# Performance work log

Measured on AMD Instinct MI355X. Metric: run time of the kernel, lower is better.

Reference implementation:

```python
import jax, jax.numpy as jnp
import numpy as np

B, S, D, H, F = 2, 2048, 1024, 16, 64  # batch, seq, d_model, heads, head_dim


def setup_inputs() -> dict:
    key = jax.random.key(0)
    ks = jax.random.split(key, 7)
    return {
        "q": jax.random.normal(ks[0], (B, S, D), dtype=jnp.float32),
        "k": jax.random.normal(ks[1], (B, S, D), dtype=jnp.float32),
        "v": jax.random.normal(ks[2], (B, S, D), dtype=jnp.float32),
        "Wq": jax.random.normal(ks[3], (H, D, F), dtype=jnp.float32) * 0.02,
        "Wk": jax.random.normal(ks[4], (H, D, F), dtype=jnp.float32) * 0.02,
        "Wv": jax.random.normal(ks[5], (H, D, F), dtype=jnp.float32) * 0.02,
        "Wo": jax.random.normal(ks[6], (H * F, D), dtype=jnp.float32) * 0.02,
    }


def reference(q, k, v, Wq, Wk, Wv, Wo):
    head_dim = Wq.shape[-1]
    queries = jnp.einsum('bqo,hof->bhqf', q, Wq)
    keys = jnp.einsum('bko,hof->bhkf', k, Wk)
    values = jnp.einsum('bvo,hof->bhvf', v, Wv)
    # K.batch_dot(queries, keys, axes=[3,3]) -> [b,h,q,k]
    scores = jnp.einsum('bhqf,bhkf->bhqk', queries, keys) / jnp.sqrt(
        jnp.asarray(head_dim, dtype=queries.dtype))
    attn = jax.nn.softmax(scores, axis=-1)
    # Faithful to K.batch_dot(attn, values, axes=[2,2]):
    # contracts the QUERY axis of attn with the seq axis of values -> A^T V
    out4 = jnp.einsum('bhqk,bhqf->bhkf', attn, values)  # [b,h,s,f]
    b = out4.shape[0]
    # Faithful raw reshape [b,h,s,f] -> [b,s,h*f] (no transpose, as in original)
    out = out4.reshape(b, out4.shape[2], -1)
    return out @ Wo  # [b,s,d_model]
```

## Files before the change

### kernel.cpp

```cpp
#include <hip/hip_runtime.h>
#include <stdint.h>

#define Bc 2
#define Sc 2048
#define Dc 1024
#define Hc 16
#define Fc 64
constexpr int BHSF = Bc * Hc * Sc * Fc;

typedef __attribute__((ext_vector_type(8))) short bf16x8;
typedef __attribute__((ext_vector_type(4))) short bf16x4;
typedef __attribute__((ext_vector_type(4))) float f32x4;

#define MFMA16(a, b, c) __builtin_amdgcn_mfma_f32_16x16x32_bf16(a, b, c, 0, 0, 0)
#define EXP2(x) __builtin_amdgcn_exp2f(x)
#define SCALE2 0.18033688f

__device__ inline short f2bf(float x) {
    uint32_t u = __builtin_bit_cast(uint32_t, x);
    u = (u + 0x7fffu + ((u >> 16) & 1u)) >> 16;
    return (short)u;
}

__global__ __launch_bounds__(256) void xcvt_kernel(
    const float* __restrict__ a, const float* __restrict__ b,
    const float* __restrict__ c, short* __restrict__ out)
{
    const float* src = (blockIdx.y == 0) ? a : (blockIdx.y == 1) ? b : c;
    const size_t base = (size_t)blockIdx.x * 4096 + threadIdx.x * 16;
    const float* s = src + base;
    short* d = out + (size_t)blockIdx.y * 4096 * 1024 + base;
    f32x4 v0 = ((const f32x4*)s)[0], v1 = ((const f32x4*)s)[1];
    f32x4 v2 = ((const f32x4*)s)[2], v3 = ((const f32x4*)s)[3];
    bf16x8 p0, p1;
    #pragma unroll
    for (int i = 0; i < 4; ++i) {
        p0[i] = f2bf(v0[i]); p0[4 + i] = f2bf(v1[i]);
        p1[i] = f2bf(v2[i]); p1[4 + i] = f2bf(v3[i]);
    }
    *(bf16x8*)d       = p0;
    *(bf16x8*)(d + 8) = p1;
}

__global__ __launch_bounds__(256) void tcvt3_kernel(
    const float* __restrict__ Wq, const float* __restrict__ Wk,
    const float* __restrict__ Wv,
    short* __restrict__ WqT, short* __restrict__ WkT, short* __restrict__ WvT)
{
    __shared__ short td[64 * 72];
    const int t = threadIdx.x;
    const int sr = t >> 2, sc = (t & 3) * 16;
    const int sel = blockIdx.z >> 4, h = blockIdx.z & 15;
    const int m0 = blockIdx.x * 64;
    const float* in = ((sel == 0) ? Wq : (sel == 1) ? Wk : Wv) + (size_t)h * Dc * Fc;
    short* out = ((sel == 0) ? WqT : (sel == 1) ? WkT : WvT) + (size_t)h * Fc * Dc;

    const float* src = in + (size_t)(m0 + sr) * Fc + sc;
    #pragma unroll
    for (int i = 0; i < 16; i += 4) {
        f32x4 a = *(const f32x4*)(src + i);
        td[sr * 72 + sc + i + 0] = f2bf(a[0]);
        td[sr * 72 + sc + i + 1] = f2bf(a[1]);
        td[sr * 72 + sc + i + 2] = f2bf(a[2]);
        td[sr * 72 + sc + i + 3] = f2bf(a[3]);
    }
    __syncthreads();
    alignas(16) short vals[16];
    #pragma unroll
    for (int i = 0; i < 16; ++i) vals[i] = td[(sc + i) * 72 + sr];
    short* dst = out + (size_t)sr * Dc + m0 + sc;
    *(bf16x8*)dst       = *(const bf16x8*)&vals[0];
    *(bf16x8*)(dst + 8) = *(const bf16x8*)&vals[8];
}

__global__ __launch_bounds__(256) void tcvt_kernel(
    const float* __restrict__ in, short* __restrict__ out, int M, int N)
{
    __shared__ short td[64 * 72];
    const int t = threadIdx.x;
    const int sr = t >> 2, sc = (t & 3) * 16;
    const int m0 = blockIdx.x * 64, n0 = blockIdx.y * 64;

    const float* src = in + (size_t)(m0 + sr) * N + n0 + sc;
    #pragma unroll
    for (int i = 0; i < 16; i += 4) {
        f32x4 a = *(const f32x4*)(src + i);
        td[sr * 72 + sc + i + 0] = f2bf(a[0]);
        td[sr * 72 + sc + i + 1] = f2bf(a[1]);
        td[sr * 72 + sc + i + 2] = f2bf(a[2]);
        td[sr * 72 + sc + i + 3] = f2bf(a[3]);
    }
    __syncthreads();
    alignas(16) short vals[16];
    #pragma unroll
    for (int i = 0; i < 16; ++i) vals[i] = td[(sc + i) * 72 + sr];
    short* dst = out + (size_t)(n0 + sr) * M + m0 + sc;
    *(bf16x8*)dst       = *(const bf16x8*)&vals[0];
    *(bf16x8*)(dst + 8) = *(const bf16x8*)&vals[8];
}

__global__ __launch_bounds__(256) void proj_kernel(
    const short* __restrict__ Xb,
    const short* __restrict__ WqT, const short* __restrict__ WkT,
    const short* __restrict__ WvT,
    short* __restrict__ Qo, short* __restrict__ Ko, short* __restrict__ VtO)
{
    const int z = blockIdx.z, h = blockIdx.x, mt = blockIdx.y;
    const short* X  = Xb + (size_t)z * 4096 * Dc;
    const short* Wt = ((z == 0) ? WqT : (z == 1) ? WkT : WvT) + (size_t)h * Fc * Dc;
    const int m0 = mt * 128;

    __shared__ short xsA[128 * 72], xsB[128 * 72];
    __shared__ short wsA[64 * 72],  wsB[64 * 72];

    const int t = threadIdx.x, lane = t & 63, w = t >> 6;
    const int l15 = lane & 15, g = lane >> 4;
    const int xr = t >> 1, xc = (t & 1) * 32;
    const int wr = t >> 2, wc = (t & 3) * 16;

    bf16x8 xg[4], wg[2];
    auto gload = [&](int d0) {
        const short* s = &X[(size_t)(m0 + xr) * Dc + d0 + xc];
        #pragma unroll
        for (int j = 0; j < 4; ++j) xg[j] = *(const bf16x8*)(s + 8 * j);
        const short* ww = &Wt[(size_t)wr * Dc + d0 + wc];
        wg[0] = *(const bf16x8*)ww;
        wg[1] = *(const bf16x8*)(ww + 8);
    };
    auto swrite = [&](short* xsD, short* wsD) {
        #pragma unroll
        for (int j = 0; j < 4; ++j) *(bf16x8*)&xsD[xr * 72 + xc + 8 * j] = xg[j];
        *(bf16x8*)&wsD[wr * 72 + wc]     = wg[0];
        *(bf16x8*)&wsD[wr * 72 + wc + 8] = wg[1];
    };

    f32x4 acc[2][4];
    #pragma unroll
    for (int i = 0; i < 2; ++i)
        #pragma unroll
        for (int j = 0; j < 4; ++j) acc[i][j] = (f32x4){0.f, 0.f, 0.f, 0.f};

    gload(0); swrite(xsA, wsA); gload(64);

    auto half = [&](int d0, const short* xsC, const short* wsC,
                    short* xsN, short* wsN) {
        __syncthreads();
        if (d0 + 64 < Dc) swrite(xsN, wsN);
        if (d0 + 128 < Dc) gload(d0 + 128);
        #pragma unroll
        for (int kc = 0; kc < 64; kc += 32) {
            bf16x8 afr[2], bfr[4];
            #pragma unroll
            for (int ms = 0; ms < 2; ++ms)
                afr[ms] = *(const bf16x8*)&xsC[(w * 32 + ms * 16 + l15) * 72 + kc + g * 8];
            #pragma unroll
            for (int fb = 0; fb < 4; ++fb)
                bfr[fb] = *(const bf16x8*)&wsC[(fb * 16 + l15) * 72 + kc + g * 8];
            #pragma unroll
            for (int ms = 0; ms < 2; ++ms)
                #pragma unroll
                for (int fb = 0; fb < 4; ++fb)
                    acc[ms][fb] = MFMA16(afr[ms], bfr[fb], acc[ms][fb]);
        }
    };

    for (int d0 = 0; d0 < Dc; d0 += 128) {
        half(d0,      xsA, wsA, xsB, wsB);
        half(d0 + 64, xsB, wsB, xsA, wsA);
    }

    __syncthreads();
    #pragma unroll
    for (int ms = 0; ms < 2; ++ms)
        #pragma unroll
        for (int fb = 0; fb < 4; ++fb)
            #pragma unroll
            for (int r = 0; r < 4; ++r)
                xsA[(w * 32 + ms * 16 + g * 4 + r) * 72 + fb * 16 + l15] =
                    f2bf(acc[ms][fb][r]);
    __syncthreads();

    const int b = m0 >> 11, s0 = m0 & 2047;
    if (z < 2) {
        short* outp = ((z == 0) ? Qo : Ko) + ((size_t)(b * Hc + h) * Sc + s0) * Fc;
        #pragma unroll
        for (int j = 0; j < 4; ++j)
            *(bf16x8*)&outp[(size_t)xr * Fc + xc + 8 * j] =
                *(const bf16x8*)&xsA[xr * 72 + xc + 8 * j];
    } else {
        const int fr = t >> 2, sc0 = (t & 3) * 32;
        short* o = VtO + ((size_t)(b * Hc + h) * Fc + fr) * Sc + s0 + sc0;
        alignas(16) short vals[32];
        #pragma unroll
        for (int j = 0; j < 32; ++j) vals[j] = xsA[(sc0 + j) * 72 + fr];
        #pragma unroll
        for (int j = 0; j < 4; ++j)
            *(bf16x8*)(o + 8 * j) = *(const bf16x8*)&vals[8 * j];
    }
}

__global__ __launch_bounds__(256) void stats_kernel(
    const short* __restrict__ Qg, const short* __restrict__ Kg,
    float* __restrict__ mrow)
{
    const int q0 = blockIdx.x * 128;
    const int bh = blockIdx.y;
    const short* Qb = Qg + (size_t)bh * Sc * Fc;
    const short* Kb = Kg + (size_t)bh * Sc * Fc;

    __shared__ short ksA[64 * 72], ksB[64 * 72];

    const int t = threadIdx.x, lane = t & 63, w = t >> 6;
    const int l15 = lane & 15, g = lane >> 4;
    const int sr4 = t >> 2, sc4 = (t & 3) * 16;

    bf16x8 qf[2][2];
    #pragma unroll
    for (int qs2 = 0; qs2 < 2; ++qs2)
        #pragma unroll
        for (int kc2 = 0; kc2 < 2; ++kc2)
            qf[qs2][kc2] = *(const bf16x8*)
                &Qb[(size_t)(q0 + w * 32 + qs2 * 16 + l15) * Fc + kc2 * 32 + g * 8];

    bf16x8 kr0, kr1;
    auto gload = [&](int kt) {
        const short* s = &Kb[(size_t)(kt + sr4) * Fc + sc4];
        kr0 = *(const bf16x8*)s;
        kr1 = *(const bf16x8*)(s + 8);
    };
    auto swrite = [&](short* d) {
        *(bf16x8*)&d[sr4 * 72 + sc4]     = kr0;
        *(bf16x8*)&d[sr4 * 72 + sc4 + 8] = kr1;
    };

    float m[2] = {-1e30f, -1e30f}, l[2] = {0.f, 0.f};

    gload(0); swrite(ksA); gload(64);

    auto half = [&](int kt, const short* cur, short* nxt) {
        __syncthreads();
        if (kt + 64 < Sc) swrite(nxt);
        if (kt + 128 < Sc) gload(kt + 128);
        #pragma unroll
        for (int kf = 0; kf < 4; ++kf) {
            bf16x8 a0 = *(const bf16x8*)&cur[(kf * 16 + l15) * 72 + 0  + g * 8];
            bf16x8 a1 = *(const bf16x8*)&cur[(kf * 16 + l15) * 72 + 32 + g * 8];
            #pragma unroll
            for (int qs2 = 0; qs2 < 2; ++qs2) {
                f32x4 acc = (f32x4){0.f, 0.f, 0.f, 0.f};
                acc = MFMA16(a0, qf[qs2][0], acc);
                acc = MFMA16(a1, qf[qs2][1], acc);
                float s0 = acc[0] * SCALE2, s1 = acc[1] * SCALE2;
                float s2 = acc[2] * SCALE2, s3 = acc[3] * SCALE2;
                float tm = fmaxf(fmaxf(s0, s1), fmaxf(s2, s3));
                float mn = fmaxf(m[qs2], tm);
                l[qs2] = l[qs2] * EXP2(m[qs2] - mn) + EXP2(s0 - mn) + EXP2(s1 - mn)
                                                    + EXP2(s2 - mn) + EXP2(s3 - mn);
                m[qs2] = mn;
            }
        }
    };

    for (int kt = 0; kt < Sc; kt += 128) {
        half(kt,      ksA, ksB);
        half(kt + 64, ksB, ksA);
    }

    #pragma unroll
    for (int qs2 = 0; qs2 < 2; ++qs2) {
        #pragma unroll
        for (int off = 16; off < 64; off <<= 1) {
            float om = __shfl_xor(m[qs2], off, 64);
            float ol = __shfl_xor(l[qs2], off, 64);
            float mn = fmaxf(m[qs2], om);
            l[qs2] = l[qs2] * EXP2(m[qs2] - mn) + ol * EXP2(om - mn);
            m[qs2] = mn;
        }
        if (lane < 16)
            mrow[bh * Sc + q0 + w * 32 + qs2 * 16 + l15] = m[qs2] + __log2f(l[qs2]);
    }
}

__global__ __launch_bounds__(256) void attn_kernel(
    const short* __restrict__ Qg, const short* __restrict__ Kg,
    const short* __restrict__ VtG, const float* __restrict__ mrow,
    short* __restrict__ O4)
{
    const int k0 = blockIdx.x * 128;
    const int bh = blockIdx.y;
    const short* Qb = Qg  + (size_t)bh * Sc * Fc;
    const short* Kb = Kg  + (size_t)bh * Sc * Fc;
    const short* Vb = VtG + (size_t)bh * Fc * Sc;
    const float* mb = mrow + (size_t)bh * Sc;

    __shared__ short qsA[64 * 72], qsB[64 * 72];
    __shared__ short vtA[64 * 72], vtB[64 * 72];
    __shared__ short pl[128 * 72];

    const int t = threadIdx.x, lane = t & 63, w = t >> 6;
    const int l15 = lane & 15, g = lane >> 4;
    const int sr4 = t >> 2, sc4 = (t & 3) * 16;

    bf16x8 kf[2][2];
    #pragma unroll
    for (int ks2 = 0; ks2 < 2; ++ks2)
        #pragma unroll
        for (int kc2 = 0; kc2 < 2; ++kc2)
            kf[ks2][kc2] = *(const bf16x8*)
                &Kb[(size_t)(k0 + w * 32 + ks2 * 16 + l15) * Fc + kc2 * 32 + g * 8];

    f32x4 oacc[2][4];
    #pragma unroll
    for (int i = 0; i < 2; ++i)
        #pragma unroll
        for (int j = 0; j < 4; ++j) oacc[i][j] = (f32x4){0.f, 0.f, 0.f, 0.f};

    bf16x8 qr0, qr1, vr0, vr1;
    auto gload = [&](int qn) {
        const short* s = &Qb[(size_t)(qn + sr4) * Fc + sc4];
        qr0 = *(const bf16x8*)s;
        qr1 = *(const bf16x8*)(s + 8);
        const short* v = &Vb[(size_t)sr4 * Sc + qn + sc4];
        vr0 = *(const bf16x8*)v;
        vr1 = *(const bf16x8*)(v + 8);
    };
    auto swrite = [&](short* qsD, short* vtD) {
        *(bf16x8*)&qsD[sr4 * 72 + sc4]     = qr0;
        *(bf16x8*)&qsD[sr4 * 72 + sc4 + 8] = qr1;
        *(bf16x8*)&vtD[sr4 * 72 + sc4]     = vr0;
        *(bf16x8*)&vtD[sr4 * 72 + sc4 + 8] = vr1;
    };

    gload(0); swrite(qsA, vtA); gload(64);

    auto chunk = [&](int q0, const short* qsC, const short* vtC,
                     short* qsN, short* vtN) {
        __syncthreads();
        if (q0 + 64 < Sc) swrite(qsN, vtN);
        if (q0 + 128 < Sc) gload(q0 + 128);

        f32x4 mq[4];
        #pragma unroll
        for (int qf = 0; qf < 4; ++qf)
            mq[qf] = *(const f32x4*)&mb[q0 + qf * 16 + g * 4];
        #pragma unroll
        for (int qf = 0; qf < 4; ++qf) {
            bf16x8 qa0 = *(const bf16x8*)&qsC[(qf * 16 + l15) * 72 + 0  + g * 8];
            bf16x8 qa1 = *(const bf16x8*)&qsC[(qf * 16 + l15) * 72 + 32 + g * 8];
            #pragma unroll
            for (int ks2 = 0; ks2 < 2; ++ks2) {
                f32x4 acc = (f32x4){0.f, 0.f, 0.f, 0.f};
                acc = MFMA16(qa0, kf[ks2][0], acc);
                acc = MFMA16(qa1, kf[ks2][1], acc);
                bf16x4 pv;
                #pragma unroll
                for (int r = 0; r < 4; ++r)
                    pv[r] = f2bf(EXP2(acc[r] * SCALE2 - mq[qf][r]));
                *(bf16x4*)&pl[(w * 32 + ks2 * 16 + l15) * 72 + qf * 16 + g * 4] = pv;
            }
        }
        __syncthreads();

        #pragma unroll
        for (int qc = 0; qc < 64; qc += 32) {
            bf16x8 pa[2], vbf[4];
            #pragma unroll
            for (int ks2 = 0; ks2 < 2; ++ks2)
                pa[ks2] = *(const bf16x8*)&pl[(w * 32 + ks2 * 16 + l15) * 72 + qc + g * 8];
            #pragma unroll
            for (int fb = 0; fb < 4; ++fb)
                vbf[fb] = *(const bf16x8*)&vtC[(fb * 16 + l15) * 72 + qc + g * 8];
            #pragma unroll
            for (int ks2 = 0; ks2 < 2; ++ks2)
                #pragma unroll
                for (int fb = 0; fb < 4; ++fb)
                    oacc[ks2][fb] = MFMA16(pa[ks2], vbf[fb], oacc[ks2][fb]);
        }
    };

    for (int q0 = 0; q0 < Sc; q0 += 128) {
        chunk(q0,      qsA, vtA, qsB, vtB);
        chunk(q0 + 64, qsB, vtB, qsA, vtA);
    }

    __syncthreads();
    #pragma unroll
    for (int ks2 = 0; ks2 < 2; ++ks2)
        #pragma unroll
        for (int fb = 0; fb < 4; ++fb)
            #pragma unroll
            for (int r = 0; r < 4; ++r)
                pl[(w * 32 + ks2 * 16 + g * 4 + r) * 72 + fb * 16 + l15] =
                    f2bf(oacc[ks2][fb][r]);
    __syncthreads();
    {
        const int sr2 = t >> 1, sc2 = (t & 1) * 32;
        short* o = O4 + ((size_t)bh * Sc + k0 + sr2) * Fc + sc2;
        #pragma unroll
        for (int i = 0; i < 32; i += 8)
            *(bf16x8*)&o[i] = *(const bf16x8*)&pl[sr2 * 72 + sc2 + i];
    }
}

__global__ __launch_bounds__(256) void outgemm_kernel(
    const short* __restrict__ A, const short* __restrict__ WoT,
    float* __restrict__ out)
{
    const int m0 = blockIdx.x * 128, n0 = blockIdx.y * 64;

    __shared__ short asA[128 * 72], asB[128 * 72];
    __shared__ short wsA[64 * 72],  wsB[64 * 72];

    const int t = threadIdx.x, lane = t & 63, w = t >> 6;
    const int l15 = lane & 15, g = lane >> 4;
    const int ar = t >> 1, ac = (t & 1) * 32;
    const int wr = t >> 2, wc = (t & 3) * 16;

    bf16x8 ag[4], wg[2];
    auto gload = [&](int d0) {
        const short* s = &A[(size_t)(m0 + ar) * Dc + d0 + ac];
        #pragma unroll
        for (int j = 0; j < 4; ++j) ag[j] = *(const bf16x8*)(s + 8 * j);
        const short* ww = &WoT[(size_t)(n0 + wr) * Dc + d0 + wc];
        wg[0] = *(const bf16x8*)ww;
        wg[1] = *(const bf16x8*)(ww + 8);
    };
    auto swrite = [&](short* asD, short* wsD) {
        #pragma unroll
        for (int j = 0; j < 4; ++j) *(bf16x8*)&asD[ar * 72 + ac + 8 * j] = ag[j];
        *(bf16x8*)&wsD[wr * 72 + wc]     = wg[0];
        *(bf16x8*)&wsD[wr * 72 + wc + 8] = wg[1];
    };

    f32x4 acc[2][4];
    #pragma unroll
    for (int i = 0; i < 2; ++i)
        #pragma unroll
        for (int j = 0; j < 4; ++j) acc[i][j] = (f32x4){0.f, 0.f, 0.f, 0.f};

    gload(0); swrite(asA, wsA); gload(64);

    auto half = [&](int d0, const short* asC, const short* wsC,
                    short* asN, short* wsN) {
        __syncthreads();
        if (d0 + 64 < Dc) swrite(asN, wsN);
        if (d0 + 128 < Dc) gload(d0 + 128);
        #pragma unroll
        for (int kc = 0; kc < 64; kc += 32) {
            bf16x8 afr[2], bfr[4];
            #pragma unroll
            for (int ms = 0; ms < 2; ++ms)
                afr[ms] = *(const bf16x8*)&asC[(w * 32 + ms * 16 + l15) * 72 + kc + g * 8];
            #pragma unroll
            for (int nb = 0; nb < 4; ++nb)
                bfr[nb] = *(const bf16x8*)&wsC[(nb * 16 + l15) * 72 + kc + g * 8];
            #pragma unroll
            for (int ms = 0; ms < 2; ++ms)
                #pragma unroll
                for (int nb = 0; nb < 4; ++nb)
                    acc[ms][nb] = MFMA16(afr[ms], bfr[nb], acc[ms][nb]);
        }
    };

    for (int d0 = 0; d0 < Dc; d0 += 128) {
        half(d0,      asA, wsA, asB, wsB);
        half(d0 + 64, asB, wsB, asA, wsA);
    }

    #pragma unroll
    for (int ms = 0; ms < 2; ++ms)
        #pragma unroll
        for (int nb = 0; nb < 4; ++nb)
            #pragma unroll
            for (int r = 0; r < 4; ++r)
                out[(size_t)(m0 + w * 32 + ms * 16 + g * 4 + r) * 1024
                    + n0 + nb * 16 + l15] = acc[ms][nb][r];
}

extern "C" void kernel_launch(void* const* d_in, const int* in_sizes, int n_in,
                              void* d_out, int out_size, void* d_ws, size_t ws_size,
                              hipStream_t stream) {
    (void)in_sizes; (void)n_in; (void)out_size; (void)ws_size;
    const float* q  = (const float*)d_in[0];
    const float* k  = (const float*)d_in[1];
    const float* v  = (const float*)d_in[2];
    const float* Wq = (const float*)d_in[3];
    const float* Wk = (const float*)d_in[4];
    const float* Wv = (const float*)d_in[5];
    const float* Wo = (const float*)d_in[6];
    float* out = (float*)d_out;

    short* Xb  = (short*)d_ws;
    short* Qw  = Xb  + (size_t)3 * 4096 * Dc;
    short* Kw  = Qw  + BHSF;
    short* Vt  = Kw  + BHSF;
    short* O4  = Vt  + BHSF;
    short* WqT = O4  + BHSF;
    short* WkT = WqT + Hc * Dc * Fc;
    short* WvT = WkT + Hc * Dc * Fc;
    short* WoT = WvT + Hc * Dc * Fc;
    float* mw  = (float*)(WoT + Dc * Dc);

    xcvt_kernel<<<dim3(1024, 3), 256, 0, stream>>>(q, k, v, Xb);
    tcvt3_kernel<<<dim3(16, 1, 48), 256, 0, stream>>>(Wq, Wk, Wv, WqT, WkT, WvT);
    tcvt_kernel<<<dim3(16, 16, 1), 256, 0, stream>>>(Wo, WoT, Dc, Dc);
    proj_kernel<<<dim3(16, 32, 3), 256, 0, stream>>>(Xb, WqT, WkT, WvT, Qw, Kw, Vt);
    stats_kernel<<<dim3(16, 32), 256, 0, stream>>>(Qw, Kw, mw);
    attn_kernel<<<dim3(16, 32), 256, 0, stream>>>(Qw, Kw, Vt, mw, O4);
    outgemm_kernel<<<dim3(32, 16), 256, 0, stream>>>(O4, WoT, out);
}
```

Baseline: 187.5 us.

## Fuse input conversion into projection, split attention over query halves, merge in out-GEMM

Removes the separate fp32-to-bf16 input conversion kernel: the projection kernel now reads fp32 activations directly, converts them while staging into LDS, and computes two heads per block with a 128x128 tile and K-step of 32. The attention kernel moves to 512 threads covering 256 keys per block and splits the query loop into two halves on a new grid dimension. Each half writes its own bf16 partial output, and the output GEMM sums the two partials while loading. This trades an extra partial buffer, bf16 rounding of partial sums, and single-buffered LDS with two barriers per attention step for fewer launches, more attention parallelism, and no intermediate activation copy.

```diff
diff --git a/kernel.cpp b/kernel.cpp
--- a/kernel.cpp
+++ b/kernel.cpp
@@ -21,25 +21,9 @@
     u = (u + 0x7fffu + ((u >> 16) & 1u)) >> 16;
     return (short)u;
 }
-
-__global__ __launch_bounds__(256) void xcvt_kernel(
-    const float* __restrict__ a, const float* __restrict__ b,
-    const float* __restrict__ c, short* __restrict__ out)
-{
-    const float* src = (blockIdx.y == 0) ? a : (blockIdx.y == 1) ? b : c;
-    const size_t base = (size_t)blockIdx.x * 4096 + threadIdx.x * 16;
-    const float* s = src + base;
-    short* d = out + (size_t)blockIdx.y * 4096 * 1024 + base;
-    f32x4 v0 = ((const f32x4*)s)[0], v1 = ((const f32x4*)s)[1];
-    f32x4 v2 = ((const f32x4*)s)[2], v3 = ((const f32x4*)s)[3];
-    bf16x8 p0, p1;
-    #pragma unroll
-    for (int i = 0; i < 4; ++i) {
-        p0[i] = f2bf(v0[i]); p0[4 + i] = f2bf(v1[i]);
-        p1[i] = f2bf(v2[i]); p1[4 + i] = f2bf(v3[i]);
-    }
-    *(bf16x8*)d       = p0;
-    *(bf16x8*)(d + 8) = p1;
+__device__ inline float bf2f(short s) {
+    uint32_t u = ((uint32_t)(uint16_t)s) << 16;
+    return __builtin_bit_cast(float, u);
 }
 
 __global__ __launch_bounds__(256) void tcvt3_kernel(
@@ -100,102 +84,113 @@
 }
 
 __global__ __launch_bounds__(256) void proj_kernel(
-    const short* __restrict__ Xb,
+    const float* __restrict__ xq, const float* __restrict__ xk,
+    const float* __restrict__ xv,
     const short* __restrict__ WqT, const short* __restrict__ WkT,
     const short* __restrict__ WvT,
     short* __restrict__ Qo, short* __restrict__ Ko, short* __restrict__ VtO)
 {
-    const int z = blockIdx.z, h = blockIdx.x, mt = blockIdx.y;
-    const short* X  = Xb + (size_t)z * 4096 * Dc;
-    const short* Wt = ((z == 0) ? WqT : (z == 1) ? WkT : WvT) + (size_t)h * Fc * Dc;
+    const int z = blockIdx.z, hp = blockIdx.x, mt = blockIdx.y;
+    const float* x  = (z == 0) ? xq : (z == 1) ? xk : xv;
+    const short* Wt = ((z == 0) ? WqT : (z == 1) ? WkT : WvT) + (size_t)hp * 128 * Dc;
     const int m0 = mt * 128;
 
-    __shared__ short xsA[128 * 72], xsB[128 * 72];
-    __shared__ short wsA[64 * 72],  wsB[64 * 72];
+    __shared__ short xs[2][128 * 40];
+    __shared__ short ws[2][128 * 40];
 
     const int t = threadIdx.x, lane = t & 63, w = t >> 6;
+    const int wm = w >> 1, wn = w & 1;
     const int l15 = lane & 15, g = lane >> 4;
-    const int xr = t >> 1, xc = (t & 1) * 32;
-    const int wr = t >> 2, wc = (t & 3) * 16;
-
-    bf16x8 xg[4], wg[2];
+    const int str = t >> 1, stc = (t & 1) * 16;
+
+    f32x4 xg[4]; bf16x8 wg[2];
     auto gload = [&](int d0) {
-        const short* s = &X[(size_t)(m0 + xr) * Dc + d0 + xc];
-        #pragma unroll
-        for (int j = 0; j < 4; ++j) xg[j] = *(const bf16x8*)(s + 8 * j);
-        const short* ww = &Wt[(size_t)wr * Dc + d0 + wc];
+        const float* s = &x[(size_t)(m0 + str) * Dc + d0 + stc];
+        #pragma unroll
+        for (int j = 0; j < 4; ++j) xg[j] = ((const f32x4*)s)[j];
+        const short* ww = &Wt[(size_t)str * Dc + d0 + stc];
         wg[0] = *(const bf16x8*)ww;
         wg[1] = *(const bf16x8*)(ww + 8);
     };
-    auto swrite = [&](short* xsD, short* wsD) {
-        #pragma unroll
-        for (int j = 0; j < 4; ++j) *(bf16x8*)&xsD[xr * 72 + xc + 8 * j] = xg[j];
-        *(bf16x8*)&wsD[wr * 72 + wc]     = wg[0];
-        *(bf16x8*)&wsD[wr * 72 + wc + 8] = wg[1];
-    };
-
-    f32x4 acc[2][4];
-    #pragma unroll
-    for (int i = 0; i < 2; ++i)
+    auto swrite = [&](int buf) {
+        bf16x8 p0, p1;
+        #pragma unroll
+        for (int i = 0; i < 4; ++i) {
+            p0[i] = f2bf(xg[0][i]); p0[4 + i] = f2bf(xg[1][i]);
+            p1[i] = f2bf(xg[2][i]); p1[4 + i] = f2bf(xg[3][i]);
+        }
+        *(bf16x8*)&xs[buf][str * 40 + stc]     = p0;
+        *(bf16x8*)&xs[buf][str * 40 + stc + 8] = p1;
+        *(bf16x8*)&ws[buf][str * 40 + stc]     = wg[0];
+        *(bf16x8*)&ws[buf][str * 40 + stc + 8] = wg[1];
+    };
+
+    f32x4 acc[4][4];
+    #pragma unroll
+    for (int i = 0; i < 4; ++i)
         #pragma unroll
         for (int j = 0; j < 4; ++j) acc[i][j] = (f32x4){0.f, 0.f, 0.f, 0.f};
 
-    gload(0); swrite(xsA, wsA); gload(64);
-
-    auto half = [&](int d0, const short* xsC, const short* wsC,
-                    short* xsN, short* wsN) {
+    gload(0); swrite(0); gload(32);
+
+    auto step = [&](int d0, int cur) {
         __syncthreads();
-        if (d0 + 64 < Dc) swrite(xsN, wsN);
-        if (d0 + 128 < Dc) gload(d0 + 128);
-        #pragma unroll
-        for (int kc = 0; kc < 64; kc += 32) {
-            bf16x8 afr[2], bfr[4];
-            #pragma unroll
-            for (int ms = 0; ms < 2; ++ms)
-                afr[ms] = *(const bf16x8*)&xsC[(w * 32 + ms * 16 + l15) * 72 + kc + g * 8];
+        if (d0 + 32 < Dc) swrite(cur ^ 1);
+        if (d0 + 64 < Dc) gload(d0 + 64);
+        bf16x8 afr[4], bfr[4];
+        #pragma unroll
+        for (int ms = 0; ms < 4; ++ms)
+            afr[ms] = *(const bf16x8*)&xs[cur][(wm * 64 + ms * 16 + l15) * 40 + g * 8];
+        #pragma unroll
+        for (int fb = 0; fb < 4; ++fb)
+            bfr[fb] = *(const bf16x8*)&ws[cur][(wn * 64 + fb * 16 + l15) * 40 + g * 8];
+        #pragma unroll
+        for (int ms = 0; ms < 4; ++ms)
             #pragma unroll
             for (int fb = 0; fb < 4; ++fb)
-                bfr[fb] = *(const bf16x8*)&wsC[(fb * 16 + l15) * 72 + kc + g * 8];
-            #pragma unroll
-            for (int ms = 0; ms < 2; ++ms)
+                acc[ms][fb] = MFMA16(afr[ms], bfr[fb], acc[ms][fb]);
+    };
+
+    for (int d0 = 0; d0 < Dc; d0 += 64) {
+        step(d0, 0);
+        step(d0 + 32, 1);
+    }
+
+    __syncthreads();
+    {
+        short* bb = wn ? &ws[0][0] : &xs[0][0];
+        #pragma unroll
+        for (int ms = 0; ms < 4; ++ms)
+            #pragma unroll
+            for (int fb = 0; fb < 4; ++fb)
                 #pragma unroll
-                for (int fb = 0; fb < 4; ++fb)
-                    acc[ms][fb] = MFMA16(afr[ms], bfr[fb], acc[ms][fb]);
-        }
-    };
-
-    for (int d0 = 0; d0 < Dc; d0 += 128) {
-        half(d0,      xsA, wsA, xsB, wsB);
-        half(d0 + 64, xsB, wsB, xsA, wsA);
-    }
-
-    __syncthreads();
-    #pragma unroll
-    for (int ms = 0; ms < 2; ++ms)
-        #pragma unroll
-        for (int fb = 0; fb < 4; ++fb)
-            #pragma unroll
-            for (int r = 0; r < 4; ++r)
-                xsA[(w * 32 + ms * 16 + g * 4 + r) * 72 + fb * 16 + l15] =
-                    f2bf(acc[ms][fb][r]);
+                for (int r = 0; r < 4; ++r)
+                    bb[(wm * 64 + ms * 16 + g * 4 + r) * 80 + fb * 16 + l15] =
+                        f2bf(acc[ms][fb][r]);
+    }
     __syncthreads();
 
     const int b = m0 >> 11, s0 = m0 & 2047;
     if (z < 2) {
-        short* outp = ((z == 0) ? Qo : Ko) + ((size_t)(b * Hc + h) * Sc + s0) * Fc;
-        #pragma unroll
-        for (int j = 0; j < 4; ++j)
-            *(bf16x8*)&outp[(size_t)xr * Fc + xc + 8 * j] =
-                *(const bf16x8*)&xsA[xr * 72 + xc + 8 * j];
+        const int row = t & 127, half = t >> 7;
+        const short* src = (half ? &ws[0][0] : &xs[0][0]) + row * 80;
+        short* outp = ((z == 0) ? Qo : Ko)
+                    + ((size_t)(b * Hc + hp * 2 + half) * Sc + s0 + row) * Fc;
+        #pragma unroll
+        for (int j = 0; j < 64; j += 8)
+            *(bf16x8*)&outp[j] = *(const bf16x8*)&src[j];
     } else {
-        const int fr = t >> 2, sc0 = (t & 3) * 32;
-        short* o = VtO + ((size_t)(b * Hc + h) * Fc + fr) * Sc + s0 + sc0;
-        alignas(16) short vals[32];
-        #pragma unroll
-        for (int j = 0; j < 32; ++j) vals[j] = xsA[(sc0 + j) * 72 + fr];
-        #pragma unroll
-        for (int j = 0; j < 4; ++j)
-            *(bf16x8*)(o + 8 * j) = *(const bf16x8*)&vals[8 * j];
+        const int fhr = t & 127, half = fhr >> 6, f = fhr & 63;
+        const int colg = t >> 7;
+        const short* src = half ? &ws[0][0] : &xs[0][0];
+        short* o = VtO + ((size_t)(b * Hc + hp * 2 + half) * Fc + f) * Sc
+                       + s0 + colg * 64;
+        alignas(16) short vals[64];
+        #pragma unroll
+        for (int j = 0; j < 64; ++j) vals[j] = src[(colg * 64 + j) * 80 + f];
+        #pragma unroll
+        for (int j = 0; j < 64; j += 8)
+            *(bf16x8*)(o + j) = *(const bf16x8*)&vals[j];
     }
 }
 
@@ -281,25 +276,27 @@
     }
 }
 
-__global__ __launch_bounds__(256) void attn_kernel(
+__global__ __launch_bounds__(512) void attn_kernel(
     const short* __restrict__ Qg, const short* __restrict__ Kg,
     const short* __restrict__ VtG, const float* __restrict__ mrow,
-    short* __restrict__ O4)
+    short* __restrict__ O4a, short* __restrict__ O4b)
 {
-    const int k0 = blockIdx.x * 128;
-    const int bh = blockIdx.y;
+    const int k0 = blockIdx.x * 256;
+    const int qh = blockIdx.y;
+    const int bh = blockIdx.z;
+    const int qbeg = qh * 1024, qend = qbeg + 1024;
     const short* Qb = Qg  + (size_t)bh * Sc * Fc;
     const short* Kb = Kg  + (size_t)bh * Sc * Fc;
     const short* Vb = VtG + (size_t)bh * Fc * Sc;
     const float* mb = mrow + (size_t)bh * Sc;
 
-    __shared__ short qsA[64 * 72], qsB[64 * 72];
-    __shared__ short vtA[64 * 72], vtB[64 * 72];
-    __shared__ short pl[128 * 72];
+    __shared__ short qs[64 * 72];
+    __shared__ short vt[64 * 72];
+    __shared__ short pl[256 * 72];
 
     const int t = threadIdx.x, lane = t & 63, w = t >> 6;
     const int l15 = lane & 15, g = lane >> 4;
-    const int sr4 = t >> 2, sc4 = (t & 3) * 16;
+    const int sr8 = t >> 3, sc8 = (t & 7) * 8;
 
     bf16x8 kf[2][2];
     #pragma unroll
@@ -315,38 +312,29 @@
         #pragma unroll
         for (int j = 0; j < 4; ++j) oacc[i][j] = (f32x4){0.f, 0.f, 0.f, 0.f};
 
-    bf16x8 qr0, qr1, vr0, vr1;
+    bf16x8 qr, vr;
     auto gload = [&](int qn) {
-        const short* s = &Qb[(size_t)(qn + sr4) * Fc + sc4];
-        qr0 = *(const bf16x8*)s;
-        qr1 = *(const bf16x8*)(s + 8);
-        const short* v = &Vb[(size_t)sr4 * Sc + qn + sc4];
-        vr0 = *(const bf16x8*)v;
-        vr1 = *(const bf16x8*)(v + 8);
-    };
-    auto swrite = [&](short* qsD, short* vtD) {
-        *(bf16x8*)&qsD[sr4 * 72 + sc4]     = qr0;
-        *(bf16x8*)&qsD[sr4 * 72 + sc4 + 8] = qr1;
-        *(bf16x8*)&vtD[sr4 * 72 + sc4]     = vr0;
-        *(bf16x8*)&vtD[sr4 * 72 + sc4 + 8] = vr1;
-    };
-
-    gload(0); swrite(qsA, vtA); gload(64);
-
-    auto chunk = [&](int q0, const short* qsC, const short* vtC,
-                     short* qsN, short* vtN) {
+        qr = *(const bf16x8*)&Qb[(size_t)(qn + sr8) * Fc + sc8];
+        vr = *(const bf16x8*)&Vb[(size_t)sr8 * Sc + qn + sc8];
+    };
+
+    gload(qbeg);
+
+    for (int q0 = qbeg; q0 < qend; q0 += 64) {
         __syncthreads();
-        if (q0 + 64 < Sc) swrite(qsN, vtN);
-        if (q0 + 128 < Sc) gload(q0 + 128);
-
+        *(bf16x8*)&qs[sr8 * 72 + sc8] = qr;
+        *(bf16x8*)&vt[sr8 * 72 + sc8] = vr;
+        if (q0 + 64 < qend) gload(q0 + 64);
         f32x4 mq[4];
         #pragma unroll
         for (int qf = 0; qf < 4; ++qf)
             mq[qf] = *(const f32x4*)&mb[q0 + qf * 16 + g * 4];
+        __syncthreads();
+
         #pragma unroll
         for (int qf = 0; qf < 4; ++qf) {
-            bf16x8 qa0 = *(const bf16x8*)&qsC[(qf * 16 + l15) * 72 + 0  + g * 8];
-            bf16x8 qa1 = *(const bf16x8*)&qsC[(qf * 16 + l15) * 72 + 32 + g * 8];
+            bf16x8 qa0 = *(const bf16x8*)&qs[(qf * 16 + l15) * 72 + 0  + g * 8];
+            bf16x8 qa1 = *(const bf16x8*)&qs[(qf * 16 + l15) * 72 + 32 + g * 8];
             #pragma unroll
             for (int ks2 = 0; ks2 < 2; ++ks2) {
                 f32x4 acc = (f32x4){0.f, 0.f, 0.f, 0.f};
@@ -369,18 +357,13 @@
                 pa[ks2] = *(const bf16x8*)&pl[(w * 32 + ks2 * 16 + l15) * 72 + qc + g * 8];
             #pragma unroll
             for (int fb = 0; fb < 4; ++fb)
-                vbf[fb] = *(const bf16x8*)&vtC[(fb * 16 + l15) * 72 + qc + g * 8];
+                vbf[fb] = *(const bf16x8*)&vt[(fb * 16 + l15) * 72 + qc + g * 8];
             #pragma unroll
             for (int ks2 = 0; ks2 < 2; ++ks2)
                 #pragma unroll
                 for (int fb = 0; fb < 4; ++fb)
                     oacc[ks2][fb] = MFMA16(pa[ks2], vbf[fb], oacc[ks2][fb]);
         }
-    };
-
-    for (int q0 = 0; q0 < Sc; q0 += 128) {
-        chunk(q0,      qsA, vtA, qsB, vtB);
-        chunk(q0 + 64, qsB, vtB, qsA, vtA);
     }
 
     __syncthreads();
@@ -394,8 +377,9 @@
                     f2bf(oacc[ks2][fb][r]);
     __syncthreads();
     {
+        short* O = qh ? O4b : O4a;
         const int sr2 = t >> 1, sc2 = (t & 1) * 32;
-        short* o = O4 + ((size_t)bh * Sc + k0 + sr2) * Fc + sc2;
+        short* o = O + ((size_t)bh * Sc + k0 + sr2) * Fc + sc2;
         #pragma unroll
         for (int i = 0; i < 32; i += 8)
             *(bf16x8*)&o[i] = *(const bf16x8*)&pl[sr2 * 72 + sc2 + i];
@@ -403,8 +387,8 @@
 }
 
 __global__ __launch_bounds__(256) void outgemm_kernel(
-    const short* __restrict__ A, const short* __restrict__ WoT,
-    float* __restrict__ out)
+    const short* __restrict__ Aa, const short* __restrict__ Ab,
+    const short* __restrict__ WoT, float* __restrict__ out)
 {
     const int m0 = blockIdx.x * 128, n0 = blockIdx.y * 64;
 
@@ -416,18 +400,25 @@
     const int ar = t >> 1, ac = (t & 1) * 32;
     const int wr = t >> 2, wc = (t & 3) * 16;
 
-    bf16x8 ag[4], wg[2];
+    bf16x8 ag0[4], ag1[4], wg[2];
     auto gload = [&](int d0) {
-        const short* s = &A[(size_t)(m0 + ar) * Dc + d0 + ac];
-        #pragma unroll
-        for (int j = 0; j < 4; ++j) ag[j] = *(const bf16x8*)(s + 8 * j);
+        const short* s0 = &Aa[(size_t)(m0 + ar) * Dc + d0 + ac];
+        const short* s1 = &Ab[(size_t)(m0 + ar) * Dc + d0 + ac];
+        #pragma unroll
+        for (int j = 0; j < 4; ++j) { ag0[j] = *(const bf16x8*)(s0 + 8 * j);
+                                      ag1[j] = *(const bf16x8*)(s1 + 8 * j); }
         const short* ww = &WoT[(size_t)(n0 + wr) * Dc + d0 + wc];
         wg[0] = *(const bf16x8*)ww;
         wg[1] = *(const bf16x8*)(ww + 8);
     };
     auto swrite = [&](short* asD, short* wsD) {
         #pragma unroll
-        for (int j = 0; j < 4; ++j) *(bf16x8*)&asD[ar * 72 + ac + 8 * j] = ag[j];
+        for (int j = 0; j < 4; ++j) {
+            bf16x8 r;
+            #pragma unroll
+            for (int i = 0; i < 8; ++i) r[i] = f2bf(bf2f(ag0[j][i]) + bf2f(ag1[j][i]));
+            *(bf16x8*)&asD[ar * 72 + ac + 8 * j] = r;
+        }
         *(bf16x8*)&wsD[wr * 72 + wc]     = wg[0];
         *(bf16x8*)&wsD[wr * 72 + wc + 8] = wg[1];
     };
@@ -490,22 +481,21 @@
     const float* Wo = (const float*)d_in[6];
     float* out = (float*)d_out;
 
-    short* Xb  = (short*)d_ws;
-    short* Qw  = Xb  + (size_t)3 * 4096 * Dc;
+    short* Qw  = (short*)d_ws;
     short* Kw  = Qw  + BHSF;
     short* Vt  = Kw  + BHSF;
-    short* O4  = Vt  + BHSF;
-    short* WqT = O4  + BHSF;
+    short* O4a = Vt  + BHSF;
+    short* O4b = O4a + BHSF;
+    short* WqT = O4b + BHSF;
     short* WkT = WqT + Hc * Dc * Fc;
     short* WvT = WkT + Hc * Dc * Fc;
     short* WoT = WvT + Hc * Dc * Fc;
     float* mw  = (float*)(WoT + Dc * Dc);
 
-    xcvt_kernel<<<dim3(1024, 3), 256, 0, stream>>>(q, k, v, Xb);
     tcvt3_kernel<<<dim3(16, 1, 48), 256, 0, stream>>>(Wq, Wk, Wv, WqT, WkT, WvT);
     tcvt_kernel<<<dim3(16, 16, 1), 256, 0, stream>>>(Wo, WoT, Dc, Dc);
-    proj_kernel<<<dim3(16, 32, 3), 256, 0, stream>>>(Xb, WqT, WkT, WvT, Qw, Kw, Vt);
+    proj_kernel<<<dim3(8, 32, 3), 256, 0, stream>>>(q, k, v, WqT, WkT, WvT, Qw, Kw, Vt);
     stats_kernel<<<dim3(16, 32), 256, 0, stream>>>(Qw, Kw, mw);
-    attn_kernel<<<dim3(16, 32), 256, 0, stream>>>(Qw, Kw, Vt, mw, O4);
-    outgemm_kernel<<<dim3(32, 16), 256, 0, stream>>>(O4, WoT, out);
-}
+    attn_kernel<<<dim3(8, 2, 32), 512, 0, stream>>>(Qw, Kw, Vt, mw, O4a, O4b);
+    outgemm_kernel<<<dim3(32, 16), 256, 0, stream>>>(O4a, O4b, WoT, out);
+}
```

Result: slower. 194.0 us (+3.5%).
